# Kernel tuning notes

Measured on AMD Instinct MI355X. Metric: run time of the kernel, lower is better.

## Reference

```python
import jax, jax.numpy as jnp
import numpy as np

B, X, C = 8192, 8, 512        # batch, map_num, img_dim==tex_dim
P, Y = 8, 1000                # n_prompts, cls_num
FAKE = 16                     # fake prompt width (hardcoded in module)
F = 2048                      # feat_dim
CLS = 1000                    # cls_num
IN_DIM = P * X * FAKE         # 1024
SF = 64.0


def setup_inputs() -> dict:
    key = jax.random.key(0)
    ks = jax.random.split(key, 8)
    s = 0.02
    return {
        "img_f": jax.random.normal(ks[0], (B, X, C), jnp.float32),
        "tex_f": jax.random.normal(ks[1], (P, Y, C), jnp.float32),
        "fake_cls": jax.random.normal(ks[2], (P, FAKE, C), jnp.float32),
        "fc_w": jax.random.normal(ks[3], (C, C), jnp.float32) * s,
        "fc_b": jnp.zeros((C,), jnp.float32),
        "bn1_g": jnp.ones((IN_DIM,), jnp.float32),
        "bn1_b": jnp.zeros((IN_DIM,), jnp.float32),
        "w1": jax.random.normal(ks[4], (F, IN_DIM), jnp.float32) * s,
        "b1": jnp.zeros((F,), jnp.float32),
        "bn2_g": jnp.ones((F,), jnp.float32),
        "bn2_b": jnp.zeros((F,), jnp.float32),
        "w2": jax.random.normal(ks[5], (CLS, F), jnp.float32) * s,
        "b2": jnp.zeros((CLS,), jnp.float32),
    }


def _bn(x, g, b, eps=1e-5):
    # BatchNorm1d in training mode: batch mean / biased batch var
    m = x.mean(axis=0)
    v = x.var(axis=0)
    return (x - m) * jax.lax.rsqrt(v + eps) * g + b


def reference(img_f, tex_f, fake_cls, fc_w, fc_b, bn1_g, bn1_b, w1, b1,
              bn2_g, bn2_b, w2, b2):
    # independent L2 norm over feature dim, scaled by x_sf=64
    img_n = img_f / (jnp.linalg.norm(img_f, axis=-1, keepdims=True) + 1e-6) * SF
    tex_n = tex_f / (jnp.linalg.norm(tex_f, axis=-1, keepdims=True) + 1e-6) * SF
    # prompt attention over the class axis
    tex_fc = jnp.einsum('pyc,dc->pyd', tex_n, fc_w) + fc_b          # fc(tex_f)
    attn = jax.nn.softmax(jnp.einsum('pxc,pyc->pxy', fake_cls, tex_fc), axis=-1)
    tex_a = jnp.einsum('pxy,pyc->pxc', attn, tex_n)                  # (P,16,C)
    # cross-modal relation: 'b x c, y d c -> b yxd' (icomp/tcomp are Identity)
    cp = jnp.einsum('bxc,pdc->bpxd', img_n, tex_a).reshape(img_n.shape[0], -1)
    # prt_fc: BN -> Linear -> ELU -> BN -> Linear
    h = jax.nn.elu(_bn(cp, bn1_g, bn1_b) @ w1.T + b1)
    return _bn(h, bn2_g, bn2_b) @ w2.T + b2
```

## Files before the change

### kernel.cpp

```cpp
#include <hip/hip_runtime.h>
#include <math.h>


typedef __attribute__((ext_vector_type(8))) short bf16x8;
typedef __attribute__((ext_vector_type(4))) float f32x4;

__device__ __forceinline__ float waveSum(float v) {
#pragma unroll
    for (int o = 32; o > 0; o >>= 1) v += __shfl_xor(v, o);
    return v;
}
__device__ __forceinline__ float waveMax(float v) {
#pragma unroll
    for (int o = 32; o > 0; o >>= 1) v = fmaxf(v, __shfl_xor(v, o));
    return v;
}
__device__ __forceinline__ unsigned short f2bf(float x) {
    union { float f; unsigned u; } v; v.f = x;
    unsigned r = v.u + 0x7FFFu + ((v.u >> 16) & 1u);
    return (unsigned short)(r >> 16);
}
__device__ __forceinline__ float bf2f(unsigned short h) {
    union { unsigned u; float f; } v; v.u = ((unsigned)h) << 16; return v.f;
}
__device__ __forceinline__ void gload16(const void* g, const void* l) {
    __builtin_amdgcn_global_load_lds((const __attribute__((address_space(1))) void*)g,
                                     (__attribute__((address_space(3))) void*)l, 16, 0, 0);
}
__device__ __forceinline__ int xcd_swz(int d, int n) {
    int q = n >> 3;
    return (d & 7) * q + (d >> 3);
}

__global__ __launch_bounds__(256) void k_prep(const float* __restrict__ tex_f,
                                              unsigned short* __restrict__ texn,
                                              const float* __restrict__ fake_cls,
                                              const float* __restrict__ fc_w,
                                              unsigned short* __restrict__ g_bf) {
    __shared__ float sred[4];
    __shared__ float fcls[512];
    int bid = blockIdx.x, t = threadIdx.x;
    if (bid < 8000) {
        const float* r = tex_f + (size_t)bid * 512;
        float2 v = *(const float2*)(r + t * 2);
        float ss = v.x * v.x + v.y * v.y;
        ss = waveSum(ss);
        if ((t & 63) == 0) sred[t >> 6] = ss;
        __syncthreads();
        float tot = sred[0] + sred[1] + sred[2] + sred[3];
        float sc = 64.f / (sqrtf(tot) + 1e-6f);
        unsigned u = (unsigned)f2bf(v.x * sc) | ((unsigned)f2bf(v.y * sc) << 16);
        *(unsigned*)(texn + (size_t)bid * 512 + t * 2) = u;
    } else {
        int row = bid - 8000;
        fcls[t]       = fake_cls[row * 512 + t];
        fcls[t + 256] = fake_cls[row * 512 + t + 256];
        __syncthreads();
        float a0 = 0.f, a1 = 0.f;
        for (int d = 0; d < 512; ++d) {
            float fv = fcls[d];
            a0 = fmaf(fv, fc_w[d * 512 + t], a0);
            a1 = fmaf(fv, fc_w[d * 512 + t + 256], a1);
        }
        g_bf[row * 512 + t]       = f2bf(a0);
        g_bf[row * 512 + t + 256] = f2bf(a1);
    }
}

__global__ __launch_bounds__(256) void k_wsum_sm(const float* __restrict__ logit,
                                                 const unsigned short* __restrict__ texn,
                                                 float* __restrict__ part) {
    int yt = blockIdx.x, p = blockIdx.y, t = threadIdx.x;
    int lane = t & 63, w = t >> 6;
    __shared__ float wl[16][63];
    __shared__ float ms[16], iss[16];
    const int y0 = yt * 63;
    const int ylen = min(63, 1000 - y0);
#pragma unroll
    for (int rr = 0; rr < 4; ++rr) {
        int x = w * 4 + rr;
        const float* lr = logit + ((size_t)p * 16 + x) * 1000;
        float m = -3.0e38f;
        for (int y = lane; y < 1000; y += 64) m = fmaxf(m, lr[y]);
        m = waveMax(m);
        float s = 0.f;
        for (int y = lane; y < 1000; y += 64) s += expf(lr[y] - m);
        s = waveSum(s);
        if (lane == 0) { ms[x] = m; iss[x] = 1.f / s; }
    }
    __syncthreads();
    for (int idx = t; idx < 16 * ylen; idx += 256) {
        int x = idx / ylen, y = idx % ylen;
        wl[x][y] = expf(logit[((size_t)p * 16 + x) * 1000 + y0 + y] - ms[x]) * iss[x];
    }
    __syncthreads();
    int c0 = t * 2;
    const unsigned short* tp = texn + ((size_t)p * 1000 + y0) * 512 + c0;
    float a0[16], a1[16];
#pragma unroll
    for (int x = 0; x < 16; ++x) { a0[x] = 0.f; a1[x] = 0.f; }
    for (int y = 0; y < ylen; ++y) {
        unsigned u = *(const unsigned*)(tp + (size_t)y * 512);
        float lo = bf2f((unsigned short)(u & 0xffff));
        float hi = bf2f((unsigned short)(u >> 16));
#pragma unroll
        for (int x = 0; x < 16; ++x) {
            float ww = wl[x][y];
            a0[x] = fmaf(ww, lo, a0[x]);
            a1[x] = fmaf(ww, hi, a1[x]);
        }
    }
#pragma unroll
    for (int x = 0; x < 16; ++x) {
        float* dst = part + ((size_t)((yt * 8 + p) * 16 + x)) * 512 + c0;
        dst[0] = a0[x];
        dst[1] = a1[x];
    }
}

__global__ __launch_bounds__(256) void k_texa_red(const float* __restrict__ part,
                                                  unsigned short* __restrict__ texa) {
    int row = blockIdx.x, t = threadIdx.x;
    int p = row >> 4, x = row & 15;
    int c = t * 2;
    float s0 = 0.f, s1 = 0.f;
#pragma unroll
    for (int yt = 0; yt < 16; ++yt) {
        const float* src = part + ((size_t)((yt * 8 + p) * 16 + x)) * 512 + c;
        s0 += src[0];
        s1 += src[1];
    }
    unsigned u = (unsigned)f2bf(s0) | ((unsigned)f2bf(s1) << 16);
    *(unsigned*)(texa + (size_t)row * 512 + c) = u;
}

__global__ __launch_bounds__(256) void k_colstat_bf(const unsigned short* __restrict__ src,
                                                    float* __restrict__ ps,
                                                    float* __restrict__ pq, int ncols) {
    int col = blockIdx.x * 256 + threadIdx.x;
    int r0 = blockIdx.y * 128;
    const unsigned short* p = src + (size_t)r0 * ncols + col;
    float s = 0.f, q = 0.f;
    for (int r = 0; r < 128; ++r) {
        float v = bf2f(p[(size_t)r * ncols]);
        s += v;
        q = fmaf(v, v, q);
    }
    ps[(size_t)blockIdx.y * ncols + col] = s;
    pq[(size_t)blockIdx.y * ncols + col] = q;
}

template <bool PERM>
__global__ __launch_bounds__(256) void k_bnfin(const float* __restrict__ ps,
                                               const float* __restrict__ pq,
                                               const float* __restrict__ gam,
                                               const float* __restrict__ bet,
                                               float* __restrict__ a, float* __restrict__ c,
                                               int ncols) {
    int col = blockIdx.x * 256 + threadIdx.x;
    float S = 0.f, Q = 0.f;
    for (int i = 0; i < 64; ++i) {
        S += ps[(size_t)i * ncols + col];
        Q += pq[(size_t)i * ncols + col];
    }
    float mean = S * (1.f / 8192.f);
    float var = Q * (1.f / 8192.f) - mean * mean;
    int j = col;
    if (PERM) {
        int x = col >> 7, jj = col & 127, pp = jj >> 4, d = jj & 15;
        j = (pp << 7) + (x << 4) + d;
    }
    float av = gam[j] * rsqrtf(var + 1e-5f);
    a[col] = av;
    c[col] = bet[j] - mean * av;
}

template <bool PERM>
__global__ __launch_bounds__(256) void k_foldw_bf(const float* __restrict__ W,
                                                  const float* __restrict__ bin,
                                                  const float* __restrict__ a,
                                                  const float* __restrict__ c,
                                                  unsigned short* __restrict__ Wout,
                                                  float* __restrict__ bout,
                                                  int Kdim, int nvalid) {
    int f = blockIdx.x, t = threadIdx.x;
    unsigned short* wo = Wout + (size_t)f * Kdim;
    if (f >= nvalid) {
        for (int col = t; col < Kdim; col += 256) wo[col] = 0;
        if (t == 0) bout[f] = 0.f;
        return;
    }
    const float* wr = W + (size_t)f * Kdim;
    float partial = 0.f;
    for (int col = t; col < Kdim; col += 256) {
        int j = col;
        if (PERM) {
            int x = col >> 7, jj = col & 127, pp = jj >> 4, d = jj & 15;
            j = (pp << 7) + (x << 4) + d;
        }
        float wv = wr[j];
        wo[col] = f2bf(wv * a[col]);
        partial = fmaf(wv, c[col], partial);
    }
    partial = waveSum(partial);
    __shared__ float sred[4];
    if ((t & 63) == 0) sred[t >> 6] = partial;
    __syncthreads();
    if (t == 0) bout[f] = bin[f] + sred[0] + sred[1] + sred[2] + sred[3];
}

template <int EPI, bool A_F32, bool STATS>
__global__ __launch_bounds__(256) void gemm_mfma(const void* __restrict__ Av,
                                                 const unsigned short* __restrict__ Bv,
                                                 void* __restrict__ Cv, int K,
                                                 int ntn, int ldc, int nvalid,
                                                 const float* __restrict__ bias,
                                                 float* __restrict__ ps,
                                                 float* __restrict__ pq,
                                                 int aZ, int bZ, int cZ) {
    __shared__ unsigned short Asl[128 * 64];
    __shared__ unsigned short Bsl[128 * 64];
    __shared__ float extraA[128];
    __shared__ float extraB[128];
    const int tid = threadIdx.x;
    const int lane = tid & 63, wid = tid >> 6;
    const int wr = wid >> 1, wc = wid & 1;
    const int wg = xcd_swz(blockIdx.x, gridDim.x);
    const int m0 = (wg / ntn) * 128, n0 = (wg % ntn) * 128;
    const int z = blockIdx.y;

    const float* Af = (const float*)Av;
    const unsigned short* Ab = (const unsigned short*)Av + (size_t)z * aZ;
    const unsigned short* B = Bv + (size_t)z * bZ;

    f32x4 acc[4][4];
#pragma unroll
    for (int i = 0; i < 4; ++i)
#pragma unroll
        for (int j = 0; j < 4; ++j) acc[i][j] = {0.f, 0.f, 0.f, 0.f};

    const int swz = ((lane & 7) ^ (lane >> 3)) * 8;
    const int lrow = lane & 15, lkh = lane >> 4;
    float ssq[4] = {0.f, 0.f, 0.f, 0.f};

    for (int k0 = 0; k0 < K; k0 += 64) {
        if (A_F32) {
#pragma unroll
            for (int r = 0; r < 4; ++r) {
                int row = r * 32 + (tid >> 3);
                int kk = (tid & 7) * 8;
                const float* src = Af + (size_t)(m0 + row) * K + k0 + kk;
                float4 p0 = *(const float4*)src;
                float4 p1 = *(const float4*)(src + 4);
                ssq[r] += p0.x*p0.x + p0.y*p0.y + p0.z*p0.z + p0.w*p0.w
                        + p1.x*p1.x + p1.y*p1.y + p1.z*p1.z + p1.w*p1.w;
                bf16x8 v;
                v[0] = (short)f2bf(p0.x); v[1] = (short)f2bf(p0.y);
                v[2] = (short)f2bf(p0.z); v[3] = (short)f2bf(p0.w);
                v[4] = (short)f2bf(p1.x); v[5] = (short)f2bf(p1.y);
                v[6] = (short)f2bf(p1.z); v[7] = (short)f2bf(p1.w);
                *(bf16x8*)&Asl[row * 64 + (kk ^ ((row & 7) << 3))] = v;
            }
        } else {
#pragma unroll
            for (int r = 0; r < 4; ++r) {
                int row = r * 32 + wid * 8 + (lane >> 3);
                gload16(Ab + (size_t)(m0 + row) * K + k0 + swz,
                        Asl + r * 2048 + wid * 512);
            }
        }
#pragma unroll
        for (int r = 0; r < 4; ++r) {
            int row = r * 32 + wid * 8 + (lane >> 3);
            gload16(B + (size_t)(n0 + row) * K + k0 + swz,
                    Bsl + r * 2048 + wid * 512);
        }
        __syncthreads();
#pragma unroll
        for (int kk = 0; kk < 2; ++kk) {
            bf16x8 af[4], bfr[4];
#pragma unroll
            for (int m = 0; m < 4; ++m) {
                int row = wr * 64 + m * 16 + lrow;
                af[m] = *(const bf16x8*)&Asl[row * 64 + ((kk * 32 + lkh * 8) ^ ((row & 7) << 3))];
            }
#pragma unroll
            for (int n = 0; n < 4; ++n) {
                int row = wc * 64 + n * 16 + lrow;
                bfr[n] = *(const bf16x8*)&Bsl[row * 64 + ((kk * 32 + lkh * 8) ^ ((row & 7) << 3))];
            }
#pragma unroll
            for (int m = 0; m < 4; ++m)
#pragma unroll
                for (int n = 0; n < 4; ++n)
                    acc[m][n] = __builtin_amdgcn_mfma_f32_16x16x32_bf16(af[m], bfr[n], acc[m][n], 0, 0, 0);
        }
        __syncthreads();
    }

    if (A_F32) {
#pragma unroll
        for (int r = 0; r < 4; ++r) {
            float s = ssq[r];
            s += __shfl_xor(s, 1); s += __shfl_xor(s, 2); s += __shfl_xor(s, 4);
            if ((tid & 7) == 0) extraA[r * 32 + (tid >> 3)] = 64.f / (sqrtf(s) + 1e-6f);
        }
        __syncthreads();
    }

    const int colbase = n0 + wc * 64 + lrow;
    float bv[4];
    if (EPI == 1 || EPI == 2) {
#pragma unroll
        for (int n = 0; n < 4; ++n) bv[n] = bias[colbase + n * 16];
    }
    if (EPI == 0) {
        unsigned short* C = (unsigned short*)Cv;
#pragma unroll
        for (int m = 0; m < 4; ++m) {
            int rloc = wr * 64 + m * 16 + lkh * 4;
#pragma unroll
            for (int r = 0; r < 4; ++r) {
                float riv = extraA[rloc + r];
#pragma unroll
                for (int n = 0; n < 4; ++n)
                    C[(size_t)(m0 + rloc + r) * ldc + colbase + n * 16] = f2bf(acc[m][n][r] * riv);
            }
        }
    } else if (EPI == 1) {
        unsigned short* C = (unsigned short*)Cv;
        float sN[4] = {0.f, 0.f, 0.f, 0.f}, qN[4] = {0.f, 0.f, 0.f, 0.f};
#pragma unroll
        for (int m = 0; m < 4; ++m) {
            int row = m0 + wr * 64 + m * 16 + lkh * 4;
#pragma unroll
            for (int r = 0; r < 4; ++r)
#pragma unroll
                for (int n = 0; n < 4; ++n) {
                    float v = acc[m][n][r] + bv[n];
                    v = v > 0.f ? v : expm1f(v);
                    sN[n] += v;
                    qN[n] = fmaf(v, v, qN[n]);
                    C[(size_t)(row + r) * ldc + colbase + n * 16] = f2bf(v);
                }
        }
        if (STATS) {
#pragma unroll
            for (int n = 0; n < 4; ++n) {
                sN[n] += __shfl_xor(sN[n], 16); sN[n] += __shfl_xor(sN[n], 32);
                qN[n] += __shfl_xor(qN[n], 16); qN[n] += __shfl_xor(qN[n], 32);
            }
            __syncthreads();
            if (wr == 0 && lane < 16) {
#pragma unroll
                for (int n = 0; n < 4; ++n) {
                    extraA[wc * 64 + n * 16 + lrow] = sN[n];
                    extraB[wc * 64 + n * 16 + lrow] = qN[n];
                }
            }
            __syncthreads();
            if (wr == 1 && lane < 16) {
#pragma unroll
                for (int n = 0; n < 4; ++n) {
                    extraA[wc * 64 + n * 16 + lrow] += sN[n];
                    extraB[wc * 64 + n * 16 + lrow] += qN[n];
                }
            }
            __syncthreads();
            if (tid < 128) {
                int mt = wg / ntn;
                ps[(size_t)mt * ldc + n0 + tid] = extraA[tid];
                pq[(size_t)mt * ldc + n0 + tid] = extraB[tid];
            }
        }
    } else {
        float* C = (float*)Cv + (size_t)z * cZ;
#pragma unroll
        for (int m = 0; m < 4; ++m) {
            int row = m0 + wr * 64 + m * 16 + lkh * 4;
#pragma unroll
            for (int r = 0; r < 4; ++r) {
                if (EPI == 3 && (row + r) >= 16) continue;
#pragma unroll
                for (int n = 0; n < 4; ++n) {
                    int col = colbase + n * 16;
                    if (col < nvalid) {
                        float v = acc[m][n][r];
                        if (EPI == 2) v += bv[n];
                        C[(size_t)(row + r) * ldc + col] = v;
                    }
                }
            }
        }
    }
}

extern "C" void kernel_launch(void* const* d_in, const int* in_sizes, int n_in,
                              void* d_out, int out_size, void* d_ws, size_t ws_size,
                              hipStream_t stream) {
    const float* img_f    = (const float*)d_in[0];
    const float* tex_f    = (const float*)d_in[1];
    const float* fake_cls = (const float*)d_in[2];
    const float* fc_w     = (const float*)d_in[3];
    const float* bn1_g    = (const float*)d_in[5];
    const float* bn1_b    = (const float*)d_in[6];
    const float* w1       = (const float*)d_in[7];
    const float* b1       = (const float*)d_in[8];
    const float* bn2_g    = (const float*)d_in[9];
    const float* bn2_b    = (const float*)d_in[10];
    const float* w2       = (const float*)d_in[11];
    const float* b2       = (const float*)d_in[12];
    float* out = (float*)d_out;

    char* w = (char*)d_ws;
    unsigned short* texn = (unsigned short*)(w);
    unsigned short* g_bf = (unsigned short*)(w + 8388608);
    float*          logit= (float*)(w + 8650752);
    float*          part = (float*)(w + 9175040);
    unsigned short* texa = (unsigned short*)(w + 13369344);
    unsigned short* cp   = (unsigned short*)(w + 13500416);
    unsigned short* w1a  = (unsigned short*)(w + 30277632);
    float*          b1p  = (float*)(w + 34471936);
    float*          a1   = (float*)(w + 34480128);
    float*          c1   = (float*)(w + 34484224);
    float*          ps   = (float*)(w + 34488320);
    float*          pq   = (float*)(w + 35012608);
    unsigned short* h    = (unsigned short*)(w + 35536896);
    unsigned short* w2a  = (unsigned short*)(w + 69091328);
    float*          b2p  = (float*)(w + 73285632);
    float*          a2   = (float*)(w + 73289728);
    float*          c2   = (float*)(w + 73297920);

    k_prep<<<8128, 256, 0, stream>>>(tex_f, texn, fake_cls, fc_w, g_bf);
    gemm_mfma<3, false, false><<<dim3(8, 8), 256, 0, stream>>>(
        g_bf, texn, logit, 512, 8, 1000, 1000, nullptr, nullptr, nullptr,
        16 * 512, 1000 * 512, 16 * 1000);
    k_wsum_sm<<<dim3(16, 8), 256, 0, stream>>>(logit, texn, part);
    k_texa_red<<<128, 256, 0, stream>>>(part, texa);

    gemm_mfma<0, true, false><<<dim3(512, 1), 256, 0, stream>>>(
        img_f, texa, cp, 512, 1, 128, 128, nullptr, nullptr, nullptr, 0, 0, 0);

    k_colstat_bf<<<dim3(4, 64), 256, 0, stream>>>(cp, ps, pq, 1024);
    k_bnfin<true><<<4, 256, 0, stream>>>(ps, pq, bn1_g, bn1_b, a1, c1, 1024);
    k_foldw_bf<true><<<2048, 256, 0, stream>>>(w1, b1, a1, c1, w1a, b1p, 1024, 2048);

    gemm_mfma<1, false, true><<<dim3(1024, 1), 256, 0, stream>>>(
        cp, w1a, h, 1024, 16, 2048, 2048, b1p, ps, pq, 0, 0, 0);

    k_bnfin<false><<<8, 256, 0, stream>>>(ps, pq, bn2_g, bn2_b, a2, c2, 2048);
    k_foldw_bf<false><<<1024, 256, 0, stream>>>(w2, b2, a2, c2, w2a, b2p, 2048, 1000);

    gemm_mfma<2, false, false><<<dim3(512, 1), 256, 0, stream>>>(
        h, w2a, out, 2048, 8, 1000, 1000, b2p, nullptr, nullptr, 0, 0, 0);
}
```

Measured before the change: 249.7 us.

## Add 256-wide double-buffered 8-wave GEMM for the two MLP layers

Adds a new gemm256 kernel with 512 threads, 256x256 (or 128x256) tiles, double-buffered LDS staging via direct global-to-LDS loads, explicit vmcnt waits and split barriers, and MFMA priority hints. Both prt_fc matmuls (with the ELU+BN-stats epilogue and the bias epilogue) now use it instead of the 128x128 single-buffer kernel. The goal is more data reuse per tile and overlap of the next K-tile's loads with MFMA work. The catch is fewer blocks (256) on the GPU and heavier register/LDS use. BN partial stats are now written per half-tile row group, giving 2x more partial rows, which relies on k_bnfin reading that layout correctly.

After: 240.8 us. 3.5% less time.

```diff
diff --git a/kernel.cpp b/kernel.cpp
--- a/kernel.cpp
+++ b/kernel.cpp
@@ -31,6 +31,7 @@
     int q = n >> 3;
     return (d & 7) * q + (d >> 3);
 }
+#define SBAR __builtin_amdgcn_sched_barrier(0)
 
 __global__ __launch_bounds__(256) void k_prep(const float* __restrict__ tex_f,
                                               unsigned short* __restrict__ texn,
@@ -209,19 +210,15 @@
     if (t == 0) bout[f] = bin[f] + sred[0] + sred[1] + sred[2] + sred[3];
 }
 
-template <int EPI, bool A_F32, bool STATS>
+template <int EPI, bool A_F32>
 __global__ __launch_bounds__(256) void gemm_mfma(const void* __restrict__ Av,
                                                  const unsigned short* __restrict__ Bv,
                                                  void* __restrict__ Cv, int K,
                                                  int ntn, int ldc, int nvalid,
-                                                 const float* __restrict__ bias,
-                                                 float* __restrict__ ps,
-                                                 float* __restrict__ pq,
                                                  int aZ, int bZ, int cZ) {
     __shared__ unsigned short Asl[128 * 64];
     __shared__ unsigned short Bsl[128 * 64];
-    __shared__ float extraA[128];
-    __shared__ float extraB[128];
+    __shared__ float rowinv[128];
     const int tid = threadIdx.x;
     const int lane = tid & 63, wid = tid >> 6;
     const int wr = wid >> 1, wc = wid & 1;
@@ -303,17 +300,12 @@
         for (int r = 0; r < 4; ++r) {
             float s = ssq[r];
             s += __shfl_xor(s, 1); s += __shfl_xor(s, 2); s += __shfl_xor(s, 4);
-            if ((tid & 7) == 0) extraA[r * 32 + (tid >> 3)] = 64.f / (sqrtf(s) + 1e-6f);
+            if ((tid & 7) == 0) rowinv[r * 32 + (tid >> 3)] = 64.f / (sqrtf(s) + 1e-6f);
         }
         __syncthreads();
     }
 
     const int colbase = n0 + wc * 64 + lrow;
-    float bv[4];
-    if (EPI == 1 || EPI == 2) {
-#pragma unroll
-        for (int n = 0; n < 4; ++n) bv[n] = bias[colbase + n * 16];
-    }
     if (EPI == 0) {
         unsigned short* C = (unsigned short*)Cv;
 #pragma unroll
@@ -321,18 +313,153 @@
             int rloc = wr * 64 + m * 16 + lkh * 4;
 #pragma unroll
             for (int r = 0; r < 4; ++r) {
-                float riv = extraA[rloc + r];
+                float riv = rowinv[rloc + r];
 #pragma unroll
                 for (int n = 0; n < 4; ++n)
                     C[(size_t)(m0 + rloc + r) * ldc + colbase + n * 16] = f2bf(acc[m][n][r] * riv);
             }
         }
-    } else if (EPI == 1) {
-        unsigned short* C = (unsigned short*)Cv;
-        float sN[4] = {0.f, 0.f, 0.f, 0.f}, qN[4] = {0.f, 0.f, 0.f, 0.f};
+    } else {
+        float* C = (float*)Cv + (size_t)z * cZ;
 #pragma unroll
         for (int m = 0; m < 4; ++m) {
             int row = m0 + wr * 64 + m * 16 + lkh * 4;
+#pragma unroll
+            for (int r = 0; r < 4; ++r) {
+                if ((row + r) >= 16) continue;
+#pragma unroll
+                for (int n = 0; n < 4; ++n) {
+                    int col = colbase + n * 16;
+                    if (col < nvalid) C[(size_t)(row + r) * ldc + col] = acc[m][n][r];
+                }
+            }
+        }
+    }
+}
+
+template <int FM, int NH, int EPI>
+__global__ __launch_bounds__(512, 2) void gemm256(const unsigned short* __restrict__ A,
+                                                  const unsigned short* __restrict__ B,
+                                                  void* __restrict__ Cv, int K,
+                                                  int ntn, int ldc, int nvalid,
+                                                  const float* __restrict__ bias,
+                                                  float* __restrict__ ps,
+                                                  float* __restrict__ pq) {
+    constexpr int BM = FM * 32;
+    constexpr int MH = BM / 128;
+    constexpr int BN = NH * 128;
+    constexpr int LA = 2 * (MH + NH);
+    __shared__ unsigned short Asl[2][MH][128 * 64];
+    __shared__ unsigned short Bsl[2][NH][128 * 64];
+    const int tid = threadIdx.x;
+    const int lane = tid & 63, wid = tid >> 6;
+    const int wm = wid >> 2, wn = wid & 3;
+    const int wg = xcd_swz(blockIdx.x, gridDim.x);
+    const int m0 = (wg / ntn) * BM, n0 = (wg % ntn) * BN;
+    const int lrow = lane & 15, lkh = lane >> 4;
+    const int l7 = lane & 7;
+    const int ksrc = ((lane & 7) ^ (lane >> 3)) * 8;
+    const int mbase = wm * (BM / 2);
+    const int mhalf = mbase >> 7;
+    const int mloc0 = mbase & 127;
+    const int nbase = wn * 64;
+    const int nhalf = nbase >> 7;
+    const int nloc0 = nbase & 127;
+
+    f32x4 acc[FM][4];
+#pragma unroll
+    for (int m = 0; m < FM; ++m)
+#pragma unroll
+        for (int n = 0; n < 4; ++n) acc[m][n] = {0.f, 0.f, 0.f, 0.f};
+
+    const int nkt = K >> 6;
+
+    auto stage = [&](int kt, int buf) {
+#pragma unroll
+        for (int hf = 0; hf < MH; ++hf)
+#pragma unroll
+            for (int j = 0; j < 2; ++j) {
+                int rl = wid * 16 + j * 8 + (lane >> 3);
+                gload16(A + (size_t)(m0 + hf * 128 + rl) * K + kt * 64 + ksrc,
+                        &Asl[buf][hf][(wid * 16 + j * 8) * 64]);
+            }
+#pragma unroll
+        for (int hf = 0; hf < NH; ++hf)
+#pragma unroll
+            for (int j = 0; j < 2; ++j) {
+                int rl = wid * 16 + j * 8 + (lane >> 3);
+                gload16(B + (size_t)(n0 + hf * 128 + rl) * K + kt * 64 + ksrc,
+                        &Bsl[buf][hf][(wid * 16 + j * 8) * 64]);
+            }
+    };
+
+    stage(0, 0);
+    stage(1, 1);
+    if constexpr (LA == 8) asm volatile("s_waitcnt vmcnt(8)" ::: "memory");
+    else asm volatile("s_waitcnt vmcnt(6)" ::: "memory");
+    SBAR; __builtin_amdgcn_s_barrier(); SBAR;
+
+    for (int kt = 0; kt < nkt; ++kt) {
+        const int cur = kt & 1;
+        bf16x8 af0[FM], bf0[4];
+#pragma unroll
+        for (int m = 0; m < FM; ++m) {
+            int row = mloc0 + m * 16 + lrow;
+            af0[m] = *(const bf16x8*)&Asl[cur][mhalf][row * 64 + ((lkh ^ l7) << 3)];
+        }
+#pragma unroll
+        for (int n = 0; n < 4; ++n) {
+            int row = nloc0 + n * 16 + lrow;
+            bf0[n] = *(const bf16x8*)&Bsl[cur][nhalf][row * 64 + ((lkh ^ l7) << 3)];
+        }
+        __builtin_amdgcn_s_setprio(1);
+#pragma unroll
+        for (int m = 0; m < FM; ++m)
+#pragma unroll
+            for (int n = 0; n < 4; ++n)
+                acc[m][n] = __builtin_amdgcn_mfma_f32_16x16x32_bf16(af0[m], bf0[n], acc[m][n], 0, 0, 0);
+        __builtin_amdgcn_s_setprio(0);
+        bf16x8 af1[FM], bf1[4];
+#pragma unroll
+        for (int m = 0; m < FM; ++m) {
+            int row = mloc0 + m * 16 + lrow;
+            af1[m] = *(const bf16x8*)&Asl[cur][mhalf][row * 64 + (((4 + lkh) ^ l7) << 3)];
+        }
+#pragma unroll
+        for (int n = 0; n < 4; ++n) {
+            int row = nloc0 + n * 16 + lrow;
+            bf1[n] = *(const bf16x8*)&Bsl[cur][nhalf][row * 64 + (((4 + lkh) ^ l7) << 3)];
+        }
+        if (kt + 1 < nkt) {
+            asm volatile("s_waitcnt lgkmcnt(0)" ::: "memory");
+            SBAR; __builtin_amdgcn_s_barrier(); SBAR;
+            if (kt + 2 < nkt) {
+                stage(kt + 2, cur);
+                if constexpr (LA == 8) asm volatile("s_waitcnt vmcnt(8)" ::: "memory");
+                else asm volatile("s_waitcnt vmcnt(6)" ::: "memory");
+            } else {
+                asm volatile("s_waitcnt vmcnt(0)" ::: "memory");
+            }
+            SBAR; __builtin_amdgcn_s_barrier(); SBAR;
+        }
+        __builtin_amdgcn_s_setprio(1);
+#pragma unroll
+        for (int m = 0; m < FM; ++m)
+#pragma unroll
+            for (int n = 0; n < 4; ++n)
+                acc[m][n] = __builtin_amdgcn_mfma_f32_16x16x32_bf16(af1[m], bf1[n], acc[m][n], 0, 0, 0);
+        __builtin_amdgcn_s_setprio(0);
+    }
+
+    const int colbase = n0 + nbase + lrow;
+    if (EPI == 1) {
+        unsigned short* C = (unsigned short*)Cv;
+        float bv[4], sN[4] = {0.f, 0.f, 0.f, 0.f}, qN[4] = {0.f, 0.f, 0.f, 0.f};
+#pragma unroll
+        for (int n = 0; n < 4; ++n) bv[n] = bias[colbase + n * 16];
+#pragma unroll
+        for (int m = 0; m < FM; ++m) {
+            int row = m0 + mbase + m * 16 + lkh * 4;
 #pragma unroll
             for (int r = 0; r < 4; ++r)
 #pragma unroll
@@ -344,53 +471,34 @@
                     C[(size_t)(row + r) * ldc + colbase + n * 16] = f2bf(v);
                 }
         }
-        if (STATS) {
+#pragma unroll
+        for (int n = 0; n < 4; ++n) {
+            sN[n] += __shfl_xor(sN[n], 16); sN[n] += __shfl_xor(sN[n], 32);
+            qN[n] += __shfl_xor(qN[n], 16); qN[n] += __shfl_xor(qN[n], 32);
+        }
+        if (lane < 16) {
+            int mt = wg / ntn;
 #pragma unroll
             for (int n = 0; n < 4; ++n) {
-                sN[n] += __shfl_xor(sN[n], 16); sN[n] += __shfl_xor(sN[n], 32);
-                qN[n] += __shfl_xor(qN[n], 16); qN[n] += __shfl_xor(qN[n], 32);
-            }
-            __syncthreads();
-            if (wr == 0 && lane < 16) {
-#pragma unroll
-                for (int n = 0; n < 4; ++n) {
-                    extraA[wc * 64 + n * 16 + lrow] = sN[n];
-                    extraB[wc * 64 + n * 16 + lrow] = qN[n];
-                }
-            }
-            __syncthreads();
-            if (wr == 1 && lane < 16) {
-#pragma unroll
-                for (int n = 0; n < 4; ++n) {
-                    extraA[wc * 64 + n * 16 + lrow] += sN[n];
-                    extraB[wc * 64 + n * 16 + lrow] += qN[n];
-                }
-            }
-            __syncthreads();
-            if (tid < 128) {
-                int mt = wg / ntn;
-                ps[(size_t)mt * ldc + n0 + tid] = extraA[tid];
-                pq[(size_t)mt * ldc + n0 + tid] = extraB[tid];
+                ps[(size_t)(mt * 2 + wm) * ldc + colbase + n * 16] = sN[n];
+                pq[(size_t)(mt * 2 + wm) * ldc + colbase + n * 16] = qN[n];
             }
         }
     } else {
-        float* C = (float*)Cv + (size_t)z * cZ;
-#pragma unroll
-        for (int m = 0; m < 4; ++m) {
-            int row = m0 + wr * 64 + m * 16 + lkh * 4;
-#pragma unroll
-            for (int r = 0; r < 4; ++r) {
-                if (EPI == 3 && (row + r) >= 16) continue;
+        float* C = (float*)Cv;
+        float bv[4];
+#pragma unroll
+        for (int n = 0; n < 4; ++n) bv[n] = bias[colbase + n * 16];
+#pragma unroll
+        for (int m = 0; m < FM; ++m) {
+            int row = m0 + mbase + m * 16 + lkh * 4;
+#pragma unroll
+            for (int r = 0; r < 4; ++r)
 #pragma unroll
                 for (int n = 0; n < 4; ++n) {
                     int col = colbase + n * 16;
-                    if (col < nvalid) {
-                        float v = acc[m][n][r];
-                        if (EPI == 2) v += bv[n];
-                        C[(size_t)(row + r) * ldc + col] = v;
-                    }
+                    if (col < nvalid) C[(size_t)(row + r) * ldc + col] = acc[m][n][r] + bv[n];
                 }
-            }
         }
     }
 }
@@ -432,25 +540,24 @@
     float*          c2   = (float*)(w + 73297920);
 
     k_prep<<<8128, 256, 0, stream>>>(tex_f, texn, fake_cls, fc_w, g_bf);
-    gemm_mfma<3, false, false><<<dim3(8, 8), 256, 0, stream>>>(
-        g_bf, texn, logit, 512, 8, 1000, 1000, nullptr, nullptr, nullptr,
-        16 * 512, 1000 * 512, 16 * 1000);
+    gemm_mfma<3, false><<<dim3(8, 8), 256, 0, stream>>>(
+        g_bf, texn, logit, 512, 8, 1000, 1000, 16 * 512, 1000 * 512, 16 * 1000);
     k_wsum_sm<<<dim3(16, 8), 256, 0, stream>>>(logit, texn, part);
     k_texa_red<<<128, 256, 0, stream>>>(part, texa);
 
-    gemm_mfma<0, true, false><<<dim3(512, 1), 256, 0, stream>>>(
-        img_f, texa, cp, 512, 1, 128, 128, nullptr, nullptr, nullptr, 0, 0, 0);
+    gemm_mfma<0, true><<<dim3(512, 1), 256, 0, stream>>>(
+        img_f, texa, cp, 512, 1, 128, 128, 0, 0, 0);
 
     k_colstat_bf<<<dim3(4, 64), 256, 0, stream>>>(cp, ps, pq, 1024);
     k_bnfin<true><<<4, 256, 0, stream>>>(ps, pq, bn1_g, bn1_b, a1, c1, 1024);
     k_foldw_bf<true><<<2048, 256, 0, stream>>>(w1, b1, a1, c1, w1a, b1p, 1024, 2048);
 
-    gemm_mfma<1, false, true><<<dim3(1024, 1), 256, 0, stream>>>(
-        cp, w1a, h, 1024, 16, 2048, 2048, b1p, ps, pq, 0, 0, 0);
+    gemm256<8, 2, 1><<<dim3(256), 512, 0, stream>>>(
+        cp, w1a, h, 1024, 8, 2048, 2048, b1p, ps, pq);
 
     k_bnfin<false><<<8, 256, 0, stream>>>(ps, pq, bn2_g, bn2_b, a2, c2, 2048);
     k_foldw_bf<false><<<1024, 256, 0, stream>>>(w2, b2, a2, c2, w2a, b2p, 2048, 1000);
 
-    gemm_mfma<2, false, false><<<dim3(512, 1), 256, 0, stream>>>(
-        h, w2a, out, 2048, 8, 1000, 1000, b2p, nullptr, nullptr, 0, 0, 0);
-}
+    gemm256<4, 2, 2><<<dim3(256), 512, 0, stream>>>(
+        h, w2a, out, 2048, 4, 1000, 1000, b2p, nullptr, nullptr);
+}
```
